# Performance work log

Measured on AMD Instinct MI355X. Metric: run time of the kernel, lower is better.

The kernel has to match this reference:

```python
import jax, jax.numpy as jnp
import numpy as np

N = 100000
E = 1000000
F = 64
H = 64
G = 64  # number of graphs
EPS = 1e-5


def setup_inputs() -> dict:
    key = jax.random.key(0)
    ks = jax.random.split(key, 12)
    x = jax.random.normal(ks[0], (N, F), dtype=jnp.float32)
    edge_index = jax.random.randint(ks[1], (2, E), 0, N, dtype=jnp.int32)
    batch = jnp.sort(jax.random.randint(ks[2], (N,), 0, G, dtype=jnp.int32))
    s1 = 1.0 / np.sqrt(F)
    s2 = 1.0 / np.sqrt(H)
    inp = {
        "x": x,
        "edge_index": edge_index,
        "batch": batch,
        # GCNConv layers (weight [out,in] like torch Linear, bias [out])
        "W1": jax.random.uniform(ks[3], (H, F), jnp.float32, -s1, s1),
        "b1": jnp.zeros((H,), jnp.float32),
        "W2": jax.random.uniform(ks[4], (H, H), jnp.float32, -s2, s2),
        "b2": jnp.zeros((H,), jnp.float32),
        # BatchNorm (eval mode: running stats)
        "bn1_g": jnp.ones((H,), jnp.float32),
        "bn1_b": jnp.zeros((H,), jnp.float32),
        "bn1_m": jax.random.normal(ks[5], (H,), jnp.float32) * 0.1,
        "bn1_v": jax.random.uniform(ks[6], (H,), jnp.float32, 0.5, 1.5),
        "bn2_g": jnp.ones((H,), jnp.float32),
        "bn2_b": jnp.zeros((H,), jnp.float32),
        "bn2_m": jax.random.normal(ks[7], (H,), jnp.float32) * 0.1,
        "bn2_v": jax.random.uniform(ks[8], (H,), jnp.float32, 0.5, 1.5),
        # MLP head
        "lin1_W": jax.random.uniform(ks[9], (H // 2, H), jnp.float32, -s2, s2),
        "lin1_b": jnp.zeros((H // 2,), jnp.float32),
        "lin2_W": jax.random.uniform(ks[10], (1, H // 2), jnp.float32, -1.0 / np.sqrt(H // 2), 1.0 / np.sqrt(H // 2)),
        "lin2_b": jnp.zeros((1,), jnp.float32),
    }
    return inp


def _gcn_norm(edge_index):
    # PyG GCNConv default: add self-loops, symmetric normalization
    loop = jnp.arange(N, dtype=edge_index.dtype)
    row = jnp.concatenate([edge_index[0], loop])  # source
    col = jnp.concatenate([edge_index[1], loop])  # target
    deg = jax.ops.segment_sum(jnp.ones_like(col, jnp.float32), col, num_segments=N)
    dinv = jnp.where(deg > 0, jax.lax.rsqrt(deg), 0.0)
    norm = dinv[row] * dinv[col]  # [E+N]
    return row, col, norm


def _gcn_conv(x, W, b, row, col, norm):
    h = x @ W.T                       # [N, H] transform first (cheap)
    msg = h[row] * norm[:, None]      # [E+N, H] gather + scale
    out = jax.ops.segment_sum(msg, col, num_segments=N)  # scatter-add
    return out + b


def _bn_eval(x, g, b, m, v):
    return (x - m) * (g * jax.lax.rsqrt(v + EPS)) + b


def reference(x, edge_index, batch, W1, b1, W2, b2,
              bn1_g, bn1_b, bn1_m, bn1_v, bn2_g, bn2_b, bn2_m, bn2_v,
              lin1_W, lin1_b, lin2_W, lin2_b):
    row, col, norm = _gcn_norm(edge_index)
    # layer 1: conv -> BN -> relu (dropout inactive in eval)
    h = _gcn_conv(x, W1, b1, row, col, norm)
    h = jax.nn.relu(_bn_eval(h, bn1_g, bn1_b, bn1_m, bn1_v))
    # layer 2
    h = _gcn_conv(h, W2, b2, row, col, norm)
    h = jax.nn.relu(_bn_eval(h, bn2_g, bn2_b, bn2_m, bn2_v))
    # global mean pool over graphs
    sums = jax.ops.segment_sum(h, batch, num_segments=G)          # [G, H]
    cnt = jax.ops.segment_sum(jnp.ones((N,), h.dtype), batch, num_segments=G)
    pooled = sums / jnp.maximum(cnt, 1.0)[:, None]
    # MLP head
    z = jax.nn.relu(pooled @ lin1_W.T + lin1_b)
    return z @ lin2_W.T + lin2_b  # [G, 1]
```

## Files before the change

### kernel.cpp

```cpp
#include <hip/hip_runtime.h>
#include <math.h>

#define EPS_BN 1e-5f
#define CAP 48
#define BINSHIFT 9
#define EDGESHIFT 12
#define NBUCK_MAX 199

__device__ __forceinline__ float4 pull_fixed_d(const float4* __restrict__ h4, const float* __restrict__ dinv,
                                               const int* __restrict__ icnt, const int* __restrict__ csr,
                                               int i, int q) {
    int deg = icnt[i];
    float di = dinv[i];
    float4 acc = h4[i * 16 + q];
    float dd = di * di;
    acc.x *= dd; acc.y *= dd; acc.z *= dd; acc.w *= dd;
    int degc = min(deg, CAP);
    int base = i * CAP;
    int kend = base + ((degc + 3) & ~3);
    if (base < kend) {
        int4 rr = *(const int4*)(csr + base);
        for (int k = base; k < kend; k += 4) {
            int4 cur = rr;
            if (k + 4 < kend) rr = *(const int4*)(csr + k + 4);
            float w0 = dinv[cur.x] * di;
            float w1 = dinv[cur.y] * di;
            float w2 = dinv[cur.z] * di;
            float w3 = dinv[cur.w] * di;
            float4 v0 = h4[cur.x * 16 + q];
            float4 v1 = h4[cur.y * 16 + q];
            float4 v2 = h4[cur.z * 16 + q];
            float4 v3 = h4[cur.w * 16 + q];
            acc.x += v0.x * w0 + v1.x * w1 + v2.x * w2 + v3.x * w3;
            acc.y += v0.y * w0 + v1.y * w1 + v2.y * w2 + v3.y * w3;
            acc.z += v0.z * w0 + v1.z * w1 + v2.z * w2 + v3.z * w3;
            acc.w += v0.w * w0 + v1.w * w1 + v2.w * w2 + v3.w * w3;
        }
    }
    return acc;
}

__device__ __forceinline__ float4 pull_plain_d(const float4* __restrict__ h4, const int* __restrict__ icnt,
                                               const float* __restrict__ dinv,
                                               const int* __restrict__ csr, int i, int q) {
    int deg = icnt[i];
    float4 acc = h4[i * 16 + q];
    int degc = min(deg, CAP);
    int base = i * CAP;
    int kend = base + ((degc + 3) & ~3);
    if (base < kend) {
        int4 rr = *(const int4*)(csr + base);
        for (int k = base; k < kend; k += 4) {
            int4 cur = rr;
            if (k + 4 < kend) rr = *(const int4*)(csr + k + 4);
            float4 v0 = h4[cur.x * 16 + q];
            float4 v1 = h4[cur.y * 16 + q];
            float4 v2 = h4[cur.z * 16 + q];
            float4 v3 = h4[cur.w * 16 + q];
            acc.x += v0.x + v1.x + v2.x + v3.x;
            acc.y += v0.y + v1.y + v2.y + v3.y;
            acc.z += v0.z + v1.z + v2.z + v3.z;
            acc.w += v0.w + v1.w + v2.w + v3.w;
        }
    }
    float di = dinv[i];
    acc.x *= di; acc.y *= di; acc.z *= di; acc.w *= di;
    return acc;
}

__device__ __forceinline__ void gemm_tile128(const float4* __restrict__ in4, float4* sx, const float4* Wl,
                                             float4* __restrict__ out4, int n, int tile, int tid) {
    int rbase = tile * 128;
#pragma unroll
    for (int k = 0; k < 8; ++k) {
        int idx = tid + k * 256;
        int r = idx >> 4, c = idx & 15;
        int gr = rbase + r;
        float4 v = (gr < n) ? in4[gr * 16 + c] : float4{0.f, 0.f, 0.f, 0.f};
        sx[(r << 4) | (c ^ ((r >> 1) & 15))] = v;
    }
    __syncthreads();

    int hg = tid >> 6;
    int h0 = hg * 16;
    int ng = tid & 63;
    int n0 = rbase + 2 * ng;
    int sw = ng & 15;
    float acc[2][16];
#pragma unroll
    for (int j = 0; j < 2; ++j)
#pragma unroll
        for (int k = 0; k < 16; ++k) acc[j][k] = 0.0f;

    for (int f4 = 0; f4 < 16; ++f4) {
        float4 xv[2];
#pragma unroll
        for (int j = 0; j < 2; ++j) xv[j] = sx[((2 * ng + j) << 4) | (f4 ^ sw)];
#pragma unroll
        for (int hh = 0; hh < 16; ++hh) {
            float4 w = Wl[(h0 + hh) * 16 + f4];
#pragma unroll
            for (int j = 0; j < 2; ++j) {
                acc[j][hh] += xv[j].x * w.x;
                acc[j][hh] += xv[j].y * w.y;
                acc[j][hh] += xv[j].z * w.z;
                acc[j][hh] += xv[j].w * w.w;
            }
        }
    }
#pragma unroll
    for (int j = 0; j < 2; ++j) {
        if (n0 + j >= n) continue;
#pragma unroll
        for (int q = 0; q < 4; ++q) {
            float4 o = {acc[j][4 * q], acc[j][4 * q + 1], acc[j][4 * q + 2], acc[j][4 * q + 3]};
            out4[(n0 + j) * 16 + (h0 >> 2) + q] = o;
        }
    }
}

__global__ __launch_bounds__(256) void k_initgemm1bin(int nbg, int nblka,
    const float* __restrict__ in, const float* __restrict__ W, float* __restrict__ out, int n,
    const int* __restrict__ row, const int* __restrict__ col, int e, int nbuck,
    int2* __restrict__ regions, int* __restrict__ offs,
    int* icnt, float* dinv, float* gsum, float* gcnt, float* rowA, float* rowB,
    const float* b1, const float* g1, const float* bb1, const float* m1, const float* v1,
    const float* b2, const float* g2, const float* bb2, const float* m2, const float* v2,
    float* sc1, float* sh1, float* sc2, float* sh2) {
    __shared__ __align__(16) char smem[49152];
    int t = threadIdx.x;
    if ((int)blockIdx.x < nbg) {
        float4* sx = (float4*)smem;
        float4* Wl = (float4*)(smem + 32768);
        const float4* W4 = (const float4*)W;
        for (int i = t; i < 1024; i += 256) Wl[i] = W4[i];
        gemm_tile128((const float4*)in, sx, Wl, (float4*)out, n, blockIdx.x, t);
    } else if ((int)blockIdx.x < nbg + nblka) {
        int2* so = (int2*)smem;
        int* soff = (int*)(smem + 32768);
        int* sfill = soff + 256;
        int blk = blockIdx.x - nbg;
        int base = blk << EDGESHIFT;
        int nE = min(1 << EDGESHIFT, e - base);

        int r4[16], c4[16];
        int j0 = t * 16;
        int m = nE - j0; m = m < 0 ? 0 : (m > 16 ? 16 : m);
        if (m == 16) {
#pragma unroll
            for (int cc = 0; cc < 4; ++cc) {
                int4 a = *(const int4*)(row + base + j0 + 4 * cc);
                int4 b = *(const int4*)(col + base + j0 + 4 * cc);
                r4[4 * cc] = a.x; r4[4 * cc + 1] = a.y; r4[4 * cc + 2] = a.z; r4[4 * cc + 3] = a.w;
                c4[4 * cc] = b.x; c4[4 * cc + 1] = b.y; c4[4 * cc + 2] = b.z; c4[4 * cc + 3] = b.w;
            }
        } else {
            for (int j = 0; j < m; ++j) { r4[j] = row[base + j0 + j]; c4[j] = col[base + j0 + j]; }
        }
        if (t < nbuck) { soff[t] = 0; sfill[t] = 0; }
        __syncthreads();
        for (int j = 0; j < m; ++j) atomicAdd(&soff[c4[j] >> BINSHIFT], 1);
        __syncthreads();
        for (int d = 1; d < nbuck; d <<= 1) {
            int add = 0;
            if (t < nbuck && t >= d) add = soff[t - d];
            __syncthreads();
            if (t < nbuck) soff[t] += add;
            __syncthreads();
        }
        for (int j = 0; j < m; ++j) {
            int bk = c4[j] >> BINSHIFT;
            int pos = (bk ? soff[bk - 1] : 0) + atomicAdd(&sfill[bk], 1);
            so[pos] = make_int2(r4[j], c4[j]);
        }
        __syncthreads();
        int4* gdst = (int4*)(regions + ((size_t)blk << EDGESHIFT));
        const int4* lsrc = (const int4*)so;
#pragma unroll
        for (int k = 0; k < 8; ++k) gdst[t + 256 * k] = lsrc[t + 256 * k];
        if (t <= nbuck) offs[blk * 200 + t] = (t == 0) ? 0 : soff[t - 1];
    } else {
        int gtid = (blockIdx.x - nbg - nblka) * 256 + t;
        if (gtid < 4096) gsum[gtid] = 0.0f;
        if (gtid < 64) { gcnt[gtid] = 0.0f; rowA[gtid] = 0.0f; rowB[gtid] = 0.0f; }
        if (gtid >= 64 && gtid < 68) icnt[n + gtid - 64] = 0;
        if (gtid >= 68 && gtid < 72) dinv[n + gtid - 68] = 1.0f;
        if (gtid >= 128 && gtid < 192) {
            int tt = gtid - 128;
            float s1 = g1[tt] / sqrtf(v1[tt] + EPS_BN);
            sc1[tt] = s1;
            sh1[tt] = (b1[tt] - m1[tt]) * s1 + bb1[tt];
            float s2 = g2[tt] / sqrtf(v2[tt] + EPS_BN);
            sc2[tt] = s2;
            sh2[tt] = (b2[tt] - m2[tt]) * s2 + bb2[tt];
        }
    }
}

__global__ __launch_bounds__(256) void k_build_f(
    const int2* __restrict__ regions, const int* __restrict__ offs, int nba, int n,
    int* __restrict__ icnt, float* __restrict__ dinv, int* __restrict__ csr) {
    __shared__ int lcsr[256 * CAP];
    __shared__ int lcnt[256];
    int blk = blockIdx.x;
    int b = blk >> 1, s = blk & 1;
    int node0 = (b << BINSHIFT) + s * 256;
    if (node0 >= n) return;
    int t = threadIdx.x;
    for (int idx = t; idx < 256 * CAP; idx += 256) lcsr[idx] = n;
    lcnt[t] = 0;
    __syncthreads();
    for (int r = t; r < nba; r += 256) {
        int o0 = offs[r * 200 + b];
        int o1 = offs[r * 200 + b + 1];
        const int2* reg = regions + ((size_t)r << EDGESHIFT);
        if (o0 < o1) {
            int2 eg = reg[o0];
            for (int k = o0; k < o1; ++k) {
                int2 cur = eg;
                if (k + 1 < o1) eg = reg[k + 1];
                unsigned c = (unsigned)(cur.y - node0);
                if (c < 256u) {
                    int u = atomicAdd(&lcnt[c], 1);
                    if (u < CAP) lcsr[c * CAP + u] = cur.x;
                }
            }
        }
    }
    __syncthreads();
    int nv = min(256, n - node0);
    for (int idx = t; idx < nv * CAP; idx += 256) csr[(size_t)node0 * CAP + idx] = lcsr[idx];
    if (t < nv) {
        int d = lcnt[t];
        icnt[node0 + t] = d;
        dinv[node0 + t] = rsqrtf((float)(d + 1));
    }
}

__global__ __launch_bounds__(256) void k_applygemm2(
    const float* __restrict__ h, const int* __restrict__ icnt, const float* __restrict__ dinv,
    const int* __restrict__ csr, const float* __restrict__ W,
    const float* __restrict__ scale, const float* __restrict__ shift,
    float* __restrict__ out, int n) {
    __shared__ __align__(16) char smem[49664];
    float4* sx = (float4*)smem;
    float4* Wl = (float4*)(smem + 32768);
    float4* scl = (float4*)(smem + 49152);
    float4* shl = scl + 16;
    int t = threadIdx.x;
    const float4* W4 = (const float4*)W;
    for (int i = t; i < 1024; i += 256) Wl[i] = W4[i];
    if (t < 16) {
        scl[t] = ((const float4*)scale)[t];
        shl[t] = ((const float4*)shift)[t];
    }
    int rbase = blockIdx.x * 128;
    for (int k = 0; k < 8; ++k) {
        int idx = t + k * 256;
        int r = idx >> 4, q = idx & 15;
        int i = rbase + r;
        float4 acc = {0.f, 0.f, 0.f, 0.f};
        if (i < n) acc = pull_fixed_d((const float4*)h, dinv, icnt, csr, i, q);
        sx[(r << 4) | (q ^ ((r >> 1) & 15))] = acc;
    }
    __syncthreads();
    int hg = t >> 6;
    int h0 = hg * 16;
    int ng = t & 63;
    int n0 = rbase + 2 * ng;
    int sw = ng & 15;
    float acc[2][16];
#pragma unroll
    for (int j = 0; j < 2; ++j)
#pragma unroll
        for (int k = 0; k < 16; ++k) acc[j][k] = 0.0f;
    for (int f4 = 0; f4 < 16; ++f4) {
        float4 sc = scl[f4], sh = shl[f4];
        float4 xv[2];
#pragma unroll
        for (int j = 0; j < 2; ++j) {
            float4 v = sx[((2 * ng + j) << 4) | (f4 ^ sw)];
            v.x = fmaxf(v.x * sc.x + sh.x, 0.0f);
            v.y = fmaxf(v.y * sc.y + sh.y, 0.0f);
            v.z = fmaxf(v.z * sc.z + sh.z, 0.0f);
            v.w = fmaxf(v.w * sc.w + sh.w, 0.0f);
            xv[j] = v;
        }
#pragma unroll
        for (int hh = 0; hh < 16; ++hh) {
            float4 w = Wl[(h0 + hh) * 16 + f4];
#pragma unroll
            for (int j = 0; j < 2; ++j) {
                acc[j][hh] += xv[j].x * w.x;
                acc[j][hh] += xv[j].y * w.y;
                acc[j][hh] += xv[j].z * w.z;
                acc[j][hh] += xv[j].w * w.w;
            }
        }
    }
    float4* out4 = (float4*)out;
#pragma unroll
    for (int j = 0; j < 2; ++j) {
        if (n0 + j >= n) continue;
        float di = dinv[n0 + j];
#pragma unroll
        for (int q = 0; q < 4; ++q) {
            float4 o = {acc[j][4 * q] * di, acc[j][4 * q + 1] * di,
                        acc[j][4 * q + 2] * di, acc[j][4 * q + 3] * di};
            out4[(n0 + j) * 16 + (h0 >> 2) + q] = o;
        }
    }
}

__global__ __launch_bounds__(256) void k_applypool_f(
    const float* __restrict__ h, const int* __restrict__ icnt, const float* __restrict__ dinv,
    const int* __restrict__ csr, const int* __restrict__ batch,
    const float* __restrict__ sc, const float* __restrict__ sh,
    float* gsum, float* gcnt, int n) {
    __shared__ float spart[64 * 64];
    __shared__ float scnt[64];
    int node0 = blockIdx.x * 128;
    int last = min(node0 + 127, n - 1);
    int g0 = batch[node0];
    int rc = batch[last] - g0 + 1;
    for (int idx = threadIdx.x; idx < rc * 64; idx += 256) spart[idx] = 0.0f;
    if (threadIdx.x < rc) scnt[threadIdx.x] = 0.0f;
    __syncthreads();
    int q = threadIdx.x & 15;
    float4 s4 = ((const float4*)sc)[q];
    float4 b4 = ((const float4*)sh)[q];
    for (int it = 0; it < 8; ++it) {
        int i = node0 + it * 16 + (threadIdx.x >> 4);
        if (i < n) {
            float4 acc = pull_plain_d((const float4*)h, icnt, dinv, csr, i, q);
            acc.x = fmaxf(acc.x * s4.x + b4.x, 0.0f);
            acc.y = fmaxf(acc.y * s4.y + b4.y, 0.0f);
            acc.z = fmaxf(acc.z * s4.z + b4.z, 0.0f);
            acc.w = fmaxf(acc.w * s4.w + b4.w, 0.0f);
            int gl = batch[i] - g0;
            float* pp = &spart[gl * 64 + q * 4];
            atomicAdd(pp + 0, acc.x);
            atomicAdd(pp + 1, acc.y);
            atomicAdd(pp + 2, acc.z);
            atomicAdd(pp + 3, acc.w);
            if (q == 0) atomicAdd(&scnt[gl], 1.0f);
        }
    }
    __syncthreads();
    for (int idx = threadIdx.x; idx < rc * 64; idx += 256) {
        int gl = idx >> 6, f = idx & 63;
        atomicAdd(&gsum[(g0 + gl) * 64 + f], spart[idx]);
    }
    if (threadIdx.x < rc) atomicAdd(&gcnt[g0 + threadIdx.x], scnt[threadIdx.x]);
}

__global__ void k_mlp(const float* __restrict__ gsum, const float* __restrict__ gcnt,
                      const float* __restrict__ l1W, const float* __restrict__ l1b,
                      const float* __restrict__ l2W, const float* __restrict__ l2b,
                      float* __restrict__ outp) {
    int g = threadIdx.x;
    if (g >= 64) return;
    float inv = 1.0f / fmaxf(gcnt[g], 1.0f);
    float p[64];
#pragma unroll
    for (int hh = 0; hh < 64; ++hh) p[hh] = gsum[g * 64 + hh] * inv;
    float o = l2b[0];
    for (int j = 0; j < 32; ++j) {
        float a = l1b[j];
#pragma unroll
        for (int hh = 0; hh < 64; ++hh) a += p[hh] * l1W[j * 64 + hh];
        o += fmaxf(a, 0.0f) * l2W[j];
    }
    outp[g] = o;
}

extern "C" void kernel_launch(void* const* d_in, const int* in_sizes, int n_in,
                              void* d_out, int out_size, void* d_ws, size_t ws_size,
                              hipStream_t stream) {
    const int N = in_sizes[0] / 64;
    const int E = in_sizes[1] / 2;

    const float* x    = (const float*)d_in[0];
    const int*  row   = (const int*)d_in[1];
    const int*  colp  = ((const int*)d_in[1]) + E;
    const int*  batch = (const int*)d_in[2];
    const float* W1   = (const float*)d_in[3];
    const float* b1   = (const float*)d_in[4];
    const float* W2   = (const float*)d_in[5];
    const float* b2   = (const float*)d_in[6];
    const float* bn1g = (const float*)d_in[7];
    const float* bn1b = (const float*)d_in[8];
    const float* bn1m = (const float*)d_in[9];
    const float* bn1v = (const float*)d_in[10];
    const float* bn2g = (const float*)d_in[11];
    const float* bn2b = (const float*)d_in[12];
    const float* bn2m = (const float*)d_in[13];
    const float* bn2v = (const float*)d_in[14];
    const float* l1W  = (const float*)d_in[15];
    const float* l1b  = (const float*)d_in[16];
    const float* l2W  = (const float*)d_in[17];
    const float* l2b  = (const float*)d_in[18];
    float* out = (float*)d_out;

    int* icnt = (int*)d_ws;
    float* dinv = (float*)(icnt + N + 4);
    float* sc1 = dinv + N + 4;
    float* sh1 = sc1 + 64;
    float* sc2 = sh1 + 64;
    float* sh2 = sc2 + 64;
    float* gsum = sh2 + 64;
    float* gcnt = gsum + 4096;
    int* csr = (int*)(gcnt + 64);
    float* bufA = (float*)(csr + (size_t)N * CAP);
    float* bufB = bufA + (size_t)(N + 1) * 64;

    const int NBLKA = (E + (1 << EDGESHIFT) - 1) >> EDGESHIFT;
    const int NBUCK = (N + 511) >> BINSHIFT;
    int2* regions = (int2*)bufB;
    int* offs = (int*)(regions + ((size_t)NBLKA << EDGESHIFT));

    int nbg     = (N + 127) / 128;
    int nb_apl  = (N + 127) / 128;
    int nbuild  = NBUCK * 2;

    k_initgemm1bin<<<nbg + NBLKA + 16, 256, 0, stream>>>(nbg, NBLKA, x, W1, bufA, N,
                                                         row, colp, E, NBUCK, regions, offs,
                                                         icnt, dinv, gsum, gcnt,
                                                         bufA + (size_t)N * 64, bufB + (size_t)N * 64,
                                                         b1, bn1g, bn1b, bn1m, bn1v,
                                                         b2, bn2g, bn2b, bn2m, bn2v,
                                                         sc1, sh1, sc2, sh2);
    k_build_f<<<nbuild, 256, 0, stream>>>(regions, offs, NBLKA, N, icnt, dinv, csr);
    k_applygemm2<<<nbg, 256, 0, stream>>>(bufA, icnt, dinv, csr, W2, sc1, sh1, bufB, N);
    k_applypool_f<<<nb_apl, 256, 0, stream>>>(bufB, icnt, dinv, csr, batch, sc2, sh2, gsum, gcnt, N);
    k_mlp<<<1, 64, 0, stream>>>(gsum, gcnt, l1W, l1b, l2W, l2b, out);
}
```

Measured before the change: 314.9 us.

## Move GEMM1 into CSR-build launch and halve applygemm2 tile size

The layer-1 dense transform moves out of the binning kernel and into the same launch as the CSR build, as extra blocks, so the GEMM overlaps with the build instead of the binning pass. Separately, applygemm2 now processes 64 nodes per block with one node per thread instead of 128 nodes with two per thread. This doubles the grid and cuts shared memory per block, aiming for better occupancy in the gather-heavy aggregation. The cost is less register-level reuse of weights per thread in the second GEMM.

```diff
diff --git a/kernel.cpp b/kernel.cpp
--- a/kernel.cpp
+++ b/kernel.cpp
@@ -68,78 +68,20 @@
     return acc;
 }
 
-__device__ __forceinline__ void gemm_tile128(const float4* __restrict__ in4, float4* sx, const float4* Wl,
-                                             float4* __restrict__ out4, int n, int tile, int tid) {
-    int rbase = tile * 128;
-#pragma unroll
-    for (int k = 0; k < 8; ++k) {
-        int idx = tid + k * 256;
-        int r = idx >> 4, c = idx & 15;
-        int gr = rbase + r;
-        float4 v = (gr < n) ? in4[gr * 16 + c] : float4{0.f, 0.f, 0.f, 0.f};
-        sx[(r << 4) | (c ^ ((r >> 1) & 15))] = v;
-    }
-    __syncthreads();
-
-    int hg = tid >> 6;
-    int h0 = hg * 16;
-    int ng = tid & 63;
-    int n0 = rbase + 2 * ng;
-    int sw = ng & 15;
-    float acc[2][16];
-#pragma unroll
-    for (int j = 0; j < 2; ++j)
-#pragma unroll
-        for (int k = 0; k < 16; ++k) acc[j][k] = 0.0f;
-
-    for (int f4 = 0; f4 < 16; ++f4) {
-        float4 xv[2];
-#pragma unroll
-        for (int j = 0; j < 2; ++j) xv[j] = sx[((2 * ng + j) << 4) | (f4 ^ sw)];
-#pragma unroll
-        for (int hh = 0; hh < 16; ++hh) {
-            float4 w = Wl[(h0 + hh) * 16 + f4];
-#pragma unroll
-            for (int j = 0; j < 2; ++j) {
-                acc[j][hh] += xv[j].x * w.x;
-                acc[j][hh] += xv[j].y * w.y;
-                acc[j][hh] += xv[j].z * w.z;
-                acc[j][hh] += xv[j].w * w.w;
-            }
-        }
-    }
-#pragma unroll
-    for (int j = 0; j < 2; ++j) {
-        if (n0 + j >= n) continue;
-#pragma unroll
-        for (int q = 0; q < 4; ++q) {
-            float4 o = {acc[j][4 * q], acc[j][4 * q + 1], acc[j][4 * q + 2], acc[j][4 * q + 3]};
-            out4[(n0 + j) * 16 + (h0 >> 2) + q] = o;
-        }
-    }
-}
-
-__global__ __launch_bounds__(256) void k_initgemm1bin(int nbg, int nblka,
-    const float* __restrict__ in, const float* __restrict__ W, float* __restrict__ out, int n,
+__global__ __launch_bounds__(256) void k_binit(int nblka,
     const int* __restrict__ row, const int* __restrict__ col, int e, int nbuck,
-    int2* __restrict__ regions, int* __restrict__ offs,
+    int2* __restrict__ regions, int* __restrict__ offs, int n,
     int* icnt, float* dinv, float* gsum, float* gcnt, float* rowA, float* rowB,
     const float* b1, const float* g1, const float* bb1, const float* m1, const float* v1,
     const float* b2, const float* g2, const float* bb2, const float* m2, const float* v2,
     float* sc1, float* sh1, float* sc2, float* sh2) {
-    __shared__ __align__(16) char smem[49152];
+    __shared__ __align__(16) char smem[34816];
     int t = threadIdx.x;
-    if ((int)blockIdx.x < nbg) {
-        float4* sx = (float4*)smem;
-        float4* Wl = (float4*)(smem + 32768);
-        const float4* W4 = (const float4*)W;
-        for (int i = t; i < 1024; i += 256) Wl[i] = W4[i];
-        gemm_tile128((const float4*)in, sx, Wl, (float4*)out, n, blockIdx.x, t);
-    } else if ((int)blockIdx.x < nbg + nblka) {
+    if ((int)blockIdx.x < nblka) {
         int2* so = (int2*)smem;
         int* soff = (int*)(smem + 32768);
         int* sfill = soff + 256;
-        int blk = blockIdx.x - nbg;
+        int blk = blockIdx.x;
         int base = blk << EDGESHIFT;
         int nE = min(1 << EDGESHIFT, e - base);
 
@@ -180,7 +122,7 @@
         for (int k = 0; k < 8; ++k) gdst[t + 256 * k] = lsrc[t + 256 * k];
         if (t <= nbuck) offs[blk * 200 + t] = (t == 0) ? 0 : soff[t - 1];
     } else {
-        int gtid = (blockIdx.x - nbg - nblka) * 256 + t;
+        int gtid = (blockIdx.x - nblka) * 256 + t;
         if (gtid < 4096) gsum[gtid] = 0.0f;
         if (gtid < 64) { gcnt[gtid] = 0.0f; rowA[gtid] = 0.0f; rowB[gtid] = 0.0f; }
         if (gtid >= 64 && gtid < 68) icnt[n + gtid - 64] = 0;
@@ -197,43 +139,100 @@
     }
 }
 
-__global__ __launch_bounds__(256) void k_build_f(
-    const int2* __restrict__ regions, const int* __restrict__ offs, int nba, int n,
+__global__ __launch_bounds__(256) void k_gemm1build(int nbuild,
+    const float* __restrict__ in, const float* __restrict__ W, float* __restrict__ out, int n,
+    const int2* __restrict__ regions, const int* __restrict__ offs, int nba,
     int* __restrict__ icnt, float* __restrict__ dinv, int* __restrict__ csr) {
-    __shared__ int lcsr[256 * CAP];
-    __shared__ int lcnt[256];
-    int blk = blockIdx.x;
-    int b = blk >> 1, s = blk & 1;
-    int node0 = (b << BINSHIFT) + s * 256;
-    if (node0 >= n) return;
+    __shared__ __align__(16) char smem[50176];
     int t = threadIdx.x;
-    for (int idx = t; idx < 256 * CAP; idx += 256) lcsr[idx] = n;
-    lcnt[t] = 0;
-    __syncthreads();
-    for (int r = t; r < nba; r += 256) {
-        int o0 = offs[r * 200 + b];
-        int o1 = offs[r * 200 + b + 1];
-        const int2* reg = regions + ((size_t)r << EDGESHIFT);
-        if (o0 < o1) {
-            int2 eg = reg[o0];
-            for (int k = o0; k < o1; ++k) {
-                int2 cur = eg;
-                if (k + 1 < o1) eg = reg[k + 1];
-                unsigned c = (unsigned)(cur.y - node0);
-                if (c < 256u) {
-                    int u = atomicAdd(&lcnt[c], 1);
-                    if (u < CAP) lcsr[c * CAP + u] = cur.x;
+    if ((int)blockIdx.x < nbuild) {
+        int* lcsr = (int*)smem;
+        int* lcnt = (int*)(smem + 256 * CAP * 4);
+        int blk = blockIdx.x;
+        int b = blk >> 1, s = blk & 1;
+        int node0 = (b << BINSHIFT) + s * 256;
+        if (node0 >= n) return;
+        for (int idx = t; idx < 256 * CAP; idx += 256) lcsr[idx] = n;
+        lcnt[t] = 0;
+        __syncthreads();
+        for (int r = t; r < nba; r += 256) {
+            int o0 = offs[r * 200 + b];
+            int o1 = offs[r * 200 + b + 1];
+            const int2* reg = regions + ((size_t)r << EDGESHIFT);
+            if (o0 < o1) {
+                int2 eg = reg[o0];
+                for (int k = o0; k < o1; ++k) {
+                    int2 cur = eg;
+                    if (k + 1 < o1) eg = reg[k + 1];
+                    unsigned c = (unsigned)(cur.y - node0);
+                    if (c < 256u) {
+                        int u = atomicAdd(&lcnt[c], 1);
+                        if (u < CAP) lcsr[c * CAP + u] = cur.x;
+                    }
                 }
             }
         }
-    }
-    __syncthreads();
-    int nv = min(256, n - node0);
-    for (int idx = t; idx < nv * CAP; idx += 256) csr[(size_t)node0 * CAP + idx] = lcsr[idx];
-    if (t < nv) {
-        int d = lcnt[t];
-        icnt[node0 + t] = d;
-        dinv[node0 + t] = rsqrtf((float)(d + 1));
+        __syncthreads();
+        int nv = min(256, n - node0);
+        for (int idx = t; idx < nv * CAP; idx += 256) csr[(size_t)node0 * CAP + idx] = lcsr[idx];
+        if (t < nv) {
+            int d = lcnt[t];
+            icnt[node0 + t] = d;
+            dinv[node0 + t] = rsqrtf((float)(d + 1));
+        }
+    } else {
+        float4* sx = (float4*)smem;
+        float4* Wl = (float4*)(smem + 32768);
+        const float4* W4 = (const float4*)W;
+        for (int i = t; i < 1024; i += 256) Wl[i] = W4[i];
+        int tile = blockIdx.x - nbuild;
+        int rbase = tile * 128;
+        const float4* in4 = (const float4*)in;
+#pragma unroll
+        for (int k = 0; k < 8; ++k) {
+            int idx = t + k * 256;
+            int r = idx >> 4, c = idx & 15;
+            int gr = rbase + r;
+            float4 v = (gr < n) ? in4[gr * 16 + c] : float4{0.f, 0.f, 0.f, 0.f};
+            sx[(r << 4) | (c ^ ((r >> 1) & 15))] = v;
+        }
+        __syncthreads();
+        int hg = t >> 6;
+        int h0 = hg * 16;
+        int ng = t & 63;
+        int n0 = rbase + 2 * ng;
+        int sw = ng & 15;
+        float acc[2][16];
+#pragma unroll
+        for (int j = 0; j < 2; ++j)
+#pragma unroll
+            for (int k = 0; k < 16; ++k) acc[j][k] = 0.0f;
+        for (int f4 = 0; f4 < 16; ++f4) {
+            float4 xv[2];
+#pragma unroll
+            for (int j = 0; j < 2; ++j) xv[j] = sx[((2 * ng + j) << 4) | (f4 ^ sw)];
+#pragma unroll
+            for (int hh = 0; hh < 16; ++hh) {
+                float4 w = Wl[(h0 + hh) * 16 + f4];
+#pragma unroll
+                for (int j = 0; j < 2; ++j) {
+                    acc[j][hh] += xv[j].x * w.x;
+                    acc[j][hh] += xv[j].y * w.y;
+                    acc[j][hh] += xv[j].z * w.z;
+                    acc[j][hh] += xv[j].w * w.w;
+                }
+            }
+        }
+        float4* out4 = (float4*)out;
+#pragma unroll
+        for (int j = 0; j < 2; ++j) {
+            if (n0 + j >= n) continue;
+#pragma unroll
+            for (int q = 0; q < 4; ++q) {
+                float4 o = {acc[j][4 * q], acc[j][4 * q + 1], acc[j][4 * q + 2], acc[j][4 * q + 3]};
+                out4[(n0 + j) * 16 + (h0 >> 2) + q] = o;
+            }
+        }
     }
 }
 
@@ -242,10 +241,10 @@
     const int* __restrict__ csr, const float* __restrict__ W,
     const float* __restrict__ scale, const float* __restrict__ shift,
     float* __restrict__ out, int n) {
-    __shared__ __align__(16) char smem[49664];
+    __shared__ __align__(16) char smem[33280];
     float4* sx = (float4*)smem;
-    float4* Wl = (float4*)(smem + 32768);
-    float4* scl = (float4*)(smem + 49152);
+    float4* Wl = (float4*)(smem + 16384);
+    float4* scl = (float4*)(smem + 32768);
     float4* shl = scl + 16;
     int t = threadIdx.x;
     const float4* W4 = (const float4*)W;
@@ -254,8 +253,8 @@
         scl[t] = ((const float4*)scale)[t];
         shl[t] = ((const float4*)shift)[t];
     }
-    int rbase = blockIdx.x * 128;
-    for (int k = 0; k < 8; ++k) {
+    int rbase = blockIdx.x * 64;
+    for (int k = 0; k < 4; ++k) {
         int idx = t + k * 256;
         int r = idx >> 4, q = idx & 15;
         int i = rbase + r;
@@ -267,47 +266,35 @@
     int hg = t >> 6;
     int h0 = hg * 16;
     int ng = t & 63;
-    int n0 = rbase + 2 * ng;
-    int sw = ng & 15;
-    float acc[2][16];
-#pragma unroll
-    for (int j = 0; j < 2; ++j)
-#pragma unroll
-        for (int k = 0; k < 16; ++k) acc[j][k] = 0.0f;
+    int n0 = rbase + ng;
+    int sw = (ng >> 1) & 15;
+    float acc[16];
+#pragma unroll
+    for (int k = 0; k < 16; ++k) acc[k] = 0.0f;
     for (int f4 = 0; f4 < 16; ++f4) {
         float4 sc = scl[f4], sh = shl[f4];
-        float4 xv[2];
-#pragma unroll
-        for (int j = 0; j < 2; ++j) {
-            float4 v = sx[((2 * ng + j) << 4) | (f4 ^ sw)];
-            v.x = fmaxf(v.x * sc.x + sh.x, 0.0f);
-            v.y = fmaxf(v.y * sc.y + sh.y, 0.0f);
-            v.z = fmaxf(v.z * sc.z + sh.z, 0.0f);
-            v.w = fmaxf(v.w * sc.w + sh.w, 0.0f);
-            xv[j] = v;
-        }
+        float4 v = sx[(ng << 4) | (f4 ^ sw)];
+        v.x = fmaxf(v.x * sc.x + sh.x, 0.0f);
+        v.y = fmaxf(v.y * sc.y + sh.y, 0.0f);
+        v.z = fmaxf(v.z * sc.z + sh.z, 0.0f);
+        v.w = fmaxf(v.w * sc.w + sh.w, 0.0f);
 #pragma unroll
         for (int hh = 0; hh < 16; ++hh) {
             float4 w = Wl[(h0 + hh) * 16 + f4];
-#pragma unroll
-            for (int j = 0; j < 2; ++j) {
-                acc[j][hh] += xv[j].x * w.x;
-                acc[j][hh] += xv[j].y * w.y;
-                acc[j][hh] += xv[j].z * w.z;
-                acc[j][hh] += xv[j].w * w.w;
-            }
-        }
-    }
-    float4* out4 = (float4*)out;
-#pragma unroll
-    for (int j = 0; j < 2; ++j) {
-        if (n0 + j >= n) continue;
-        float di = dinv[n0 + j];
+            acc[hh] += v.x * w.x;
+            acc[hh] += v.y * w.y;
+            acc[hh] += v.z * w.z;
+            acc[hh] += v.w * w.w;
+        }
+    }
+    if (n0 < n) {
+        float di = dinv[n0];
+        float4* out4 = (float4*)out;
 #pragma unroll
         for (int q = 0; q < 4; ++q) {
-            float4 o = {acc[j][4 * q] * di, acc[j][4 * q + 1] * di,
-                        acc[j][4 * q + 2] * di, acc[j][4 * q + 3] * di};
-            out4[(n0 + j) * 16 + (h0 >> 2) + q] = o;
+            float4 o = {acc[4 * q] * di, acc[4 * q + 1] * di,
+                        acc[4 * q + 2] * di, acc[4 * q + 3] * di};
+            out4[n0 * 16 + (h0 >> 2) + q] = o;
         }
     }
 }
@@ -420,18 +407,19 @@
     int* offs = (int*)(regions + ((size_t)NBLKA << EDGESHIFT));
 
     int nbg     = (N + 127) / 128;
+    int nb_ag2  = (N + 63) / 64;
     int nb_apl  = (N + 127) / 128;
     int nbuild  = NBUCK * 2;
 
-    k_initgemm1bin<<<nbg + NBLKA + 16, 256, 0, stream>>>(nbg, NBLKA, x, W1, bufA, N,
-                                                         row, colp, E, NBUCK, regions, offs,
-                                                         icnt, dinv, gsum, gcnt,
-                                                         bufA + (size_t)N * 64, bufB + (size_t)N * 64,
-                                                         b1, bn1g, bn1b, bn1m, bn1v,
-                                                         b2, bn2g, bn2b, bn2m, bn2v,
-                                                         sc1, sh1, sc2, sh2);
-    k_build_f<<<nbuild, 256, 0, stream>>>(regions, offs, NBLKA, N, icnt, dinv, csr);
-    k_applygemm2<<<nbg, 256, 0, stream>>>(bufA, icnt, dinv, csr, W2, sc1, sh1, bufB, N);
+    k_binit<<<NBLKA + 16, 256, 0, stream>>>(NBLKA, row, colp, E, NBUCK, regions, offs, N,
+                                            icnt, dinv, gsum, gcnt,
+                                            bufA + (size_t)N * 64, bufB + (size_t)N * 64,
+                                            b1, bn1g, bn1b, bn1m, bn1v,
+                                            b2, bn2g, bn2b, bn2m, bn2v,
+                                            sc1, sh1, sc2, sh2);
+    k_gemm1build<<<nbuild + nbg, 256, 0, stream>>>(nbuild, x, W1, bufA, N,
+                                                   regions, offs, NBLKA, icnt, dinv, csr);
+    k_applygemm2<<<nb_ag2, 256, 0, stream>>>(bufA, icnt, dinv, csr, W2, sc1, sh1, bufB, N);
     k_applypool_f<<<nb_apl, 256, 0, stream>>>(bufB, icnt, dinv, csr, batch, sc2, sh2, gsum, gcnt, N);
     k_mlp<<<1, 64, 0, stream>>>(gsum, gcnt, l1W, l1b, l2W, l2b, out);
 }
```

Measured after the change: 291.5 us. -7.4%, faster.
